# Kernel optimization log

Hardware: AMD Instinct MI355X
Metric: run time of the kernel (lower is better)

Reference implementation:

```python
import jax, jax.numpy as jnp
import numpy as np

N_RAYS = 4096
N_SAMPLES = 128
NEAR, FAR = 0.5, 4.0
BOX_MIN, BOX_MAX = -4.0, 4.0
N_LEVELS = 16
F_PER_LEVEL = 2
LOG2_T = 19
LOW_RES, HIGH_RES = 16.0, 512.0
GEO_FEAT = 15
HIDDEN = 64
HIDDEN_C = 64
IN_CH = N_LEVELS * F_PER_LEVEL      # 32 hash-grid features
IN_CH_VIEWS = 16                     # SH degree 4
OUT_CH = 4                           # 3 color channels + sigma (last)
N_APP = 64
APP_DIM = 16

PRIMES = np.array([1, 2654435761, 805459861], dtype=np.uint32)
OFFSETS = np.array([[i, j, k] for i in (0, 1) for j in (0, 1) for k in (0, 1)], dtype=np.int32)  # [8,3]

C0 = 0.28209479177387814
C1 = 0.4886025119029199
C2 = (1.0925484305920792, -1.0925484305920792, 0.31539156525252005, -1.0925484305920792, 0.5462742152960396)
C3 = (-0.5900435899266435, 2.890611442640554, -0.4570457994644658, 0.3731763325901154, -0.4570457994644658, 1.445305721320277, -0.5900435899266435)


def sh_encode(d):
    x, y, z = d[..., 0], d[..., 1], d[..., 2]
    xx, yy, zz = x * x, y * y, z * z
    xy, yz, xz = x * y, y * z, x * z
    return jnp.stack([
        C0 * jnp.ones_like(x),
        -C1 * y, C1 * z, -C1 * x,
        C2[0] * xy, C2[1] * yz, C2[2] * (2 * zz - xx - yy), C2[3] * xz, C2[4] * (xx - yy),
        C3[0] * y * (3 * xx - yy), C3[1] * xy * z, C3[2] * y * (4 * zz - xx - yy),
        C3[3] * z * (2 * zz - 3 * xx - 3 * yy), C3[4] * x * (4 * zz - xx - yy),
        C3[5] * z * (xx - yy), C3[6] * x * (xx - 3 * yy)], axis=-1)


def hash_encode(x, tables):
    # x: [N,3]; tables: [L, 2^T, F]. Multi-res hash grid with trilinear interp (Instant-NGP / HashNeRF).
    keep = jnp.all((x >= BOX_MIN) & (x <= BOX_MAX), axis=-1)
    xc = jnp.clip(x, BOX_MIN, BOX_MAX)
    b = np.exp((np.log(HIGH_RES) - np.log(LOW_RES)) / (N_LEVELS - 1))
    resolutions = jnp.asarray(np.floor(LOW_RES * b ** np.arange(N_LEVELS)), dtype=jnp.float32)
    hmask = jnp.uint32(2 ** LOG2_T - 1)
    primes = jnp.asarray(PRIMES)
    off = jnp.asarray(OFFSETS)
    off_u = off.astype(jnp.uint32)

    def level(args):
        table, res = args
        grid = (BOX_MAX - BOX_MIN) / res
        pos = (xc - BOX_MIN) / grid
        bl = jnp.floor(pos)
        frac = pos - bl                                    # [N,3]
        corners = bl.astype(jnp.uint32)[:, None, :] + off_u[None]  # [N,8,3]
        h = corners * primes                               # uint32 wraparound
        idx = (h[..., 0] ^ h[..., 1] ^ h[..., 2]) & hmask  # [N,8]
        emb = table[idx]                                   # [N,8,F]
        w = jnp.stack([1.0 - frac, frac], axis=-1)         # [N,3,2]
        cw = w[:, 0, off[:, 0]] * w[:, 1, off[:, 1]] * w[:, 2, off[:, 2]]  # [N,8]
        return jnp.einsum('nc,ncf->nf', cw, emb)           # [N,F]

    feats = jax.lax.map(level, (tables, resolutions))      # [L,N,F]
    feats = jnp.transpose(feats, (1, 0, 2)).reshape(x.shape[0], -1)
    return feats, keep


def _forward(rays, hash_tables, w_s0, w_s1, w_s2, w_c0, w_c1, w_c2, w_c3, app_table):
    R = rays.shape[0]
    rays_o, rays_d = rays[:, :3], rays[:, 3:6]
    codes = rays[:, 6].astype(jnp.int32)
    z = jnp.linspace(NEAR, FAR, N_SAMPLES)
    zvals = jax.lax.stop_gradient(jnp.broadcast_to(z, (R, N_SAMPLES)))
    samples = jax.lax.stop_gradient(rays_o[:, None, :] + rays_d[:, None, :] * z[None, :, None])  # [R,S,3]
    viewdirs = jax.lax.stop_gradient(jnp.broadcast_to(rays_d[:, None, :], (R, N_SAMPLES, 3)))

    pts = samples.reshape(-1, 3)
    dirs = viewdirs.reshape(-1, 3)
    enc_p, keep = hash_encode(pts, hash_tables)            # [N,32], [N]
    enc_d = sh_encode(dirs)                                # [N,16]

    # sigma network (bias-free, HashNeRF NeRFSmall)
    h = jax.nn.relu(enc_p @ w_s0)
    h = jax.nn.relu(h @ w_s1)
    h = h @ w_s2                                           # [N, 1+geo_feat]
    sigma = h[:, :1]
    geo = h[:, 1:]

    # color network with per-ray appearance embedding
    app = app_table[jnp.repeat(codes, N_SAMPLES)]          # [N, APP_DIM]
    c = jnp.concatenate([enc_d, geo, app], axis=-1)
    c = jax.nn.relu(c @ w_c0)
    c = jax.nn.relu(c @ w_c1)
    c = jax.nn.relu(c @ w_c2)
    c = c @ w_c3                                           # [N, OUT_CH-1]

    sigma = jnp.where(keep[:, None], sigma, 0.0)           # output[~keep_mask, -1] = 0
    raw = jnp.concatenate([c, sigma], axis=-1).reshape(R, N_SAMPLES, OUT_CH)

    # volumetric integration
    dists = jnp.concatenate([zvals[:, 1:] - zvals[:, :-1], jnp.full((R, 1), 1e10)], axis=-1)
    dists = dists * jnp.linalg.norm(rays_d, axis=-1, keepdims=True)
    sig = jax.nn.relu(raw[..., -1])
    alpha = 1.0 - jnp.exp(-sig * dists)
    trans = jnp.cumprod(jnp.concatenate([jnp.ones((R, 1)), 1.0 - alpha + 1e-10], axis=-1), axis=-1)[:, :-1]
    weights = alpha * trans                                # [R,S]
    chs = jax.nn.sigmoid(raw[..., :-1])
    chs_map = jnp.einsum('rs,rsc->rc', weights, chs)       # [R, OUT_CH-1]
    depth_map = jnp.sum(weights * zvals, axis=-1)          # [R]
    p = jnp.concatenate([weights, 1.0 - jnp.sum(weights, -1, keepdims=True) + 1e-6], axis=-1)
    p = jnp.clip(p, 1e-12, None)
    p = p / jnp.sum(p, -1, keepdims=True)
    sparsity_loss = -jnp.sum(p * jnp.log(p), axis=-1)      # [R] Categorical entropy
    return chs_map, depth_map, sparsity_loss


def setup_inputs() -> dict:
    key = jax.random.key(0)
    ks = jax.random.split(key, 12)
    rays_o = jax.random.uniform(ks[0], (N_RAYS, 3), minval=-0.5, maxval=0.5)
    d = jax.random.normal(ks[1], (N_RAYS, 3))
    rays_d = d / jnp.linalg.norm(d, axis=-1, keepdims=True)
    codes = jax.random.randint(ks[2], (N_RAYS, 1), 0, N_APP).astype(jnp.float32)
    rays = jnp.concatenate([rays_o, rays_d, codes], axis=-1)  # [R,7]
    hash_tables = (jax.random.uniform(ks[3], (N_LEVELS, 2 ** LOG2_T, F_PER_LEVEL)) * 2.0 - 1.0) * 1e-4
    def init_w(k, shape):
        return jax.random.normal(k, shape) * (1.0 / np.sqrt(shape[0]))
    w_s0 = init_w(ks[4], (IN_CH, HIDDEN))
    w_s1 = init_w(ks[5], (HIDDEN, HIDDEN))
    w_s2 = init_w(ks[6], (HIDDEN, 1 + GEO_FEAT))
    c_in = IN_CH_VIEWS + GEO_FEAT + APP_DIM
    w_c0 = init_w(ks[7], (c_in, HIDDEN_C))
    w_c1 = init_w(ks[8], (HIDDEN_C, HIDDEN_C))
    w_c2 = init_w(ks[9], (HIDDEN_C, HIDDEN_C))
    w_c3 = init_w(ks[10], (HIDDEN_C, OUT_CH - 1))
    app_table = jax.random.normal(ks[11], (N_APP, APP_DIM)) * 0.01
    return {"rays": rays, "app_code": 0, "hash_tables": hash_tables,
            "w_s0": w_s0, "w_s1": w_s1, "w_s2": w_s2,
            "w_c0": w_c0, "w_c1": w_c1, "w_c2": w_c2, "w_c3": w_c3,
            "app_table": app_table}


def reference(rays, app_code, hash_tables, w_s0, w_s1, w_s2, w_c0, w_c1, w_c2, w_c3, app_table):
    # app_code arg is ignored by the original forward (it re-reads rays[:, 6]).
    return _forward(rays, hash_tables, w_s0, w_s1, w_s2, w_c0, w_c1, w_c2, w_c3, app_table)
```

## Files before the change

kernel.cpp:

```cpp
#include <hip/hip_runtime.h>
#include <math.h>

typedef unsigned short u16;
typedef short bf16x8 __attribute__((ext_vector_type(8)));
typedef float f32x4 __attribute__((ext_vector_type(4)));

#define NRAYS 4096
#define NSAMP 128
#define NPTS (NRAYS * NSAMP)
#define TBL_MASK 0x7FFFFu
#define LVL_STRIDE (524288 * 2)

#define SB_W0H 0
#define SB_W0M 2048
#define SB_W0L 4096
#define SB_W1H 6144
#define SB_W1M 10240
#define SB_W1L 14336
#define WB_G   18432
#define WB_C0  19456
#define WB_C1  23552
#define WB_C2  27648
#define WB_C3  31744
#define RAW_OFF 131072

#define MEMBAR() asm volatile("" ::: "memory")

struct ResArr { float r[16]; };

__device__ __forceinline__ u16 f2b(float f) {
  unsigned u = __float_as_uint(f);
  unsigned r = u + 0x7FFFu + ((u >> 16) & 1u);
  return (u16)(r >> 16);
}
__device__ __forceinline__ unsigned pack2(float lo, float hi) {
  return (unsigned)f2b(lo) | ((unsigned)f2b(hi) << 16);
}
__device__ __forceinline__ float b2f(u16 u) {
  return __uint_as_float(((unsigned)u) << 16);
}
__device__ __forceinline__ void split3(float x, u16& h, u16& m, u16& l) {
  h = f2b(x);
  float r = x - b2f(h);
  m = f2b(r);
  l = f2b(r - b2f(m));
}
__device__ __forceinline__ void split8(float4 a, float4 b, bf16x8* S) {
  float v[8] = {a.x, a.y, a.z, a.w, b.x, b.y, b.z, b.w};
  #pragma unroll
  for (int e = 0; e < 8; ++e) {
    u16 h, m, l; split3(v[e], h, m, l);
    S[0][e] = (short)h; S[1][e] = (short)m; S[2][e] = (short)l;
  }
}
__device__ __forceinline__ bf16x8 tob8(float4 a, float4 b) {
  bf16x8 r;
  r[0] = (short)f2b(a.x); r[1] = (short)f2b(a.y); r[2] = (short)f2b(a.z); r[3] = (short)f2b(a.w);
  r[4] = (short)f2b(b.x); r[5] = (short)f2b(b.y); r[6] = (short)f2b(b.z); r[7] = (short)f2b(b.w);
  return r;
}
__device__ __forceinline__ float sigmoidf_(float x) { return 1.f / (1.f + expf(-x)); }

__global__ void __launch_bounds__(256)
prep_kernel(const float* __restrict__ ws0, const float* __restrict__ ws1,
            const float* __restrict__ ws2, const float* __restrict__ wc0,
            const float* __restrict__ wc1, const float* __restrict__ wc2,
            const float* __restrict__ wc3, u16* __restrict__ wb)
{
  __shared__ int P[32];
  __shared__ int Pinv[32];
  const int t = threadIdx.x;
  if (t < 64) {
    const int g = t >> 4;
    for (int tt = 0; tt < 32; ++tt) {
      bf16x8 A, B;
      #pragma unroll
      for (int e = 0; e < 8; ++e) {
        A[e] = (short)f2b((float)(g * 8 + e + 1));
        B[e] = (short)((g * 8 + e == tt) ? 0x3F80 : 0);
      }
      f32x4 c = {0.f, 0.f, 0.f, 0.f};
      c = __builtin_amdgcn_mfma_f32_16x16x32_bf16(A, B, c, 0, 0, 0);
      if (t == 0) P[tt] = (int)(c[0] + 0.5f) - 1;
    }
  }
  __syncthreads();
  if (t < 32) Pinv[t] = t;
  __syncthreads();
  if (t < 32) { int p = P[t]; if (p >= 0 && p < 32) Pinv[p] = t; }
  __syncthreads();

  for (int i = t; i < 2048; i += 256) {
    int o = i >> 5, k = i & 31, kt = Pinv[k];
    float v = ws0[kt * 64 + o];
    u16 h, m, l; split3(v, h, m, l);
    wb[SB_W0H + i] = h; wb[SB_W0M + i] = m; wb[SB_W0L + i] = l;
  }
  for (int i = t; i < 4096; i += 256) {
    int o = i >> 6, k = i & 63, kt = (k & 32) | Pinv[k & 31];
    float v = ws1[kt * 64 + o];
    u16 h, m, l; split3(v, h, m, l);
    wb[SB_W1H + i] = h; wb[SB_W1M + i] = m; wb[SB_W1L + i] = l;
  }
  for (int i = t; i < 1024; i += 256) {
    int o = i >> 6, s = i & 63, kt = (s & 32) | Pinv[s & 31];
    wb[WB_G + i] = f2b(ws2[kt * 16 + o]);
  }
  for (int i = t; i < 4096; i += 256) {
    int o = i >> 6, s = i & 63, kt = (s & 32) | Pinv[s & 31];
    float v = 0.f;
    if (kt < 16) v = wc0[kt * 64 + o];
    else if (kt >= 17 && kt <= 47) v = wc0[(kt - 1) * 64 + o];
    wb[WB_C0 + i] = f2b(v);
  }
  for (int i = t; i < 4096; i += 256) {
    int o = i >> 6, s = i & 63, kt = (s & 32) | Pinv[s & 31];
    wb[WB_C1 + i] = f2b(wc1[kt * 64 + o]);
  }
  for (int i = t; i < 4096; i += 256) {
    int o = i >> 6, s = i & 63, kt = (s & 32) | Pinv[s & 31];
    wb[WB_C2 + i] = f2b(wc2[kt * 64 + o]);
  }
  for (int i = t; i < 1024; i += 256) {
    int o = i >> 6, s = i & 63, kt = (s & 32) | Pinv[s & 31];
    wb[WB_C3 + i] = f2b(o < 3 ? wc3[kt * 3 + o] : 0.f);
  }
}

__global__ void __launch_bounds__(64, 2)
point_kernel(const float* __restrict__ rays, const float* __restrict__ tables,
             const u16* __restrict__ wb, const float* __restrict__ ws2,
             const float* __restrict__ app_table, u16* __restrict__ raw, ResArr RES)
{
  __shared__ char lds[16640];
  char* EC = lds;
  char* H1 = lds + 8192;
  char* H2 = lds + 12288;
  float* keepb = (float*)(lds + 16384);
  const int lane = threadIdx.x;
  const int pBase = blockIdx.x * 64;
  const int q = lane & 15, g = lane >> 4;
  const unsigned swzQ = (unsigned)((q & 7) << 4);
  const unsigned swzMy = (unsigned)((lane & 7) << 4);

  const int ptG = pBase + lane;
  const int r = ptG >> 7, s = ptG & (NSAMP - 1);
  const float ox = rays[r * 7 + 0], oy = rays[r * 7 + 1], oz = rays[r * 7 + 2];
  const float dx = rays[r * 7 + 3], dy = rays[r * 7 + 4], dz = rays[r * 7 + 5];
  const int code = (int)rays[r * 7 + 6];
  const float z = 0.5f + (3.5f / 127.f) * (float)s;
  const float x = fmaf(dx, z, ox), y = fmaf(dy, z, oy), w = fmaf(dz, z, oz);
  const bool keep = (x >= -4.f && x <= 4.f && y >= -4.f && y <= 4.f &&
                     w >= -4.f && w <= 4.f);
  const float xc = fminf(fmaxf(x, -4.f), 4.f);
  const float yc = fminf(fmaxf(y, -4.f), 4.f);
  const float zc = fminf(fmaxf(w, -4.f), 4.f);

  float encp[32];
  #pragma unroll
  for (int l = 0; l < 16; ++l) {
    const float res = RES.r[l];
    const float sc = res * 0.125f;
    const float px = (xc + 4.f) * sc, py = (yc + 4.f) * sc, pz = (zc + 4.f) * sc;
    const float bx = floorf(px), by = floorf(py), bz = floorf(pz);
    const float fx = px - bx, fy = py - by, fz = pz - bz;
    const unsigned ix = (unsigned)bx, iy = (unsigned)by, iz = (unsigned)bz;
    const unsigned hx0 = ix, hx1 = ix + 1u;
    const unsigned hy0 = iy * 2654435761u, hy1 = (iy + 1u) * 2654435761u;
    const unsigned hz0 = iz * 805459861u,  hz1 = (iz + 1u) * 805459861u;
    const float wx0 = 1.f - fx, wy0 = 1.f - fy, wz0 = 1.f - fz;
    const float* tl = tables + (size_t)l * LVL_STRIDE;
    float f0 = 0.f, f1 = 0.f;
    #pragma unroll
    for (int c = 0; c < 8; ++c) {
      const unsigned cx = (c >> 2) & 1, cy = (c >> 1) & 1, cz = c & 1;
      const unsigned idx = ((cx ? hx1 : hx0) ^ (cy ? hy1 : hy0) ^ (cz ? hz1 : hz0)) & TBL_MASK;
      const float cw = (cx ? fx : wx0) * (cy ? fy : wy0) * (cz ? fz : wz0);
      const float2 e = *reinterpret_cast<const float2*>(tl + (size_t)idx * 2);
      f0 = fmaf(cw, e.x, f0);
      f1 = fmaf(cw, e.y, f1);
    }
    encp[2 * l] = f0;
    encp[2 * l + 1] = f1;
  }
  #pragma unroll
  for (int c = 0; c < 8; ++c) {
    float4 u = make_float4(encp[4 * c + 0], encp[4 * c + 1], encp[4 * c + 2], encp[4 * c + 3]);
    *(float4*)(EC + lane * 128 + (((unsigned)(c * 16)) ^ swzMy)) = u;
  }
  keepb[lane] = keep ? 1.f : 0.f;
  MEMBAR();

  auto six = [&](const u16* ph, const u16* pm, const u16* pl,
                 bf16x8 bh, bf16x8 bm, bf16x8 bl, f32x4 c) -> f32x4 {
    bf16x8 Ah = *(const bf16x8*)ph, Am = *(const bf16x8*)pm, Al = *(const bf16x8*)pl;
    c = __builtin_amdgcn_mfma_f32_16x16x32_bf16(Ah, bh, c, 0, 0, 0);
    c = __builtin_amdgcn_mfma_f32_16x16x32_bf16(Am, bh, c, 0, 0, 0);
    c = __builtin_amdgcn_mfma_f32_16x16x32_bf16(Al, bh, c, 0, 0, 0);
    c = __builtin_amdgcn_mfma_f32_16x16x32_bf16(Ah, bm, c, 0, 0, 0);
    c = __builtin_amdgcn_mfma_f32_16x16x32_bf16(Am, bm, c, 0, 0, 0);
    c = __builtin_amdgcn_mfma_f32_16x16x32_bf16(Ah, bl, c, 0, 0, 0);
    return c;
  };

  float sigv[4];
  #pragma unroll
  for (int n = 0; n < 4; ++n) {
    bf16x8 B0[3];
    {
      const char* p = EC + (n * 16 + q) * 128;
      float4 a = *(const float4*)(p + (((unsigned)(g * 32)) ^ swzQ));
      float4 b = *(const float4*)(p + (((unsigned)(g * 32 + 16)) ^ swzQ));
      split8(a, b, B0);
    }
    #pragma unroll
    for (int m = 0; m < 4; ++m) {
      const int row = (m * 16 + q) * 32 + g * 8;
      f32x4 c = {0.f, 0.f, 0.f, 0.f};
      c = six(wb + SB_W0H + row, wb + SB_W0M + row, wb + SB_W0L + row,
              B0[0], B0[1], B0[2], c);
      c[0] = fmaxf(c[0], 0.f); c[1] = fmaxf(c[1], 0.f);
      c[2] = fmaxf(c[2], 0.f); c[3] = fmaxf(c[3], 0.f);
      float4 st = make_float4(c[0], c[1], c[2], c[3]);
      *(float4*)(H1 + q * 256 + (((unsigned)(m * 64 + g * 16)) ^ swzQ)) = st;
    }
    MEMBAR();

    bf16x8 B1a[3], B1b[3];
    {
      const char* p = H1 + q * 256;
      float4 a0 = *(const float4*)(p + (((unsigned)(g * 32)) ^ swzQ));
      float4 b0 = *(const float4*)(p + (((unsigned)(g * 32 + 16)) ^ swzQ));
      split8(a0, b0, B1a);
      float4 a1 = *(const float4*)(p + (((unsigned)(128 + g * 32)) ^ swzQ));
      float4 b1 = *(const float4*)(p + (((unsigned)(128 + g * 32 + 16)) ^ swzQ));
      split8(a1, b1, B1b);
    }
    #pragma unroll
    for (int m = 0; m < 4; ++m) {
      const int r0 = (m * 16 + q) * 64 + g * 8;
      const int r1 = r0 + 32;
      f32x4 c = {0.f, 0.f, 0.f, 0.f};
      c = six(wb + SB_W1H + r0, wb + SB_W1M + r0, wb + SB_W1L + r0,
              B1a[0], B1a[1], B1a[2], c);
      c = six(wb + SB_W1H + r1, wb + SB_W1M + r1, wb + SB_W1L + r1,
              B1b[0], B1b[1], B1b[2], c);
      c[0] = fmaxf(c[0], 0.f); c[1] = fmaxf(c[1], 0.f);
      c[2] = fmaxf(c[2], 0.f); c[3] = fmaxf(c[3], 0.f);
      float4 st = make_float4(c[0], c[1], c[2], c[3]);
      *(float4*)(H2 + q * 256 + (((unsigned)(m * 64 + g * 16)) ^ swzQ)) = st;
    }
    MEMBAR();

    {
      const char* p = H2 + q * 256;
      float4 a0 = *(const float4*)(p + (((unsigned)(g * 32)) ^ swzQ));
      float4 b0 = *(const float4*)(p + (((unsigned)(g * 32 + 16)) ^ swzQ));
      bf16x8 Bg0 = tob8(a0, b0);
      float4 a1 = *(const float4*)(p + (((unsigned)(128 + g * 32)) ^ swzQ));
      float4 b1 = *(const float4*)(p + (((unsigned)(128 + g * 32 + 16)) ^ swzQ));
      bf16x8 Bg1 = tob8(a1, b1);
      bf16x8 A0 = *(const bf16x8*)(wb + WB_G + q * 64 + g * 8);
      bf16x8 A1 = *(const bf16x8*)(wb + WB_G + q * 64 + 32 + g * 8);
      f32x4 cg = {0.f, 0.f, 0.f, 0.f};
      cg = __builtin_amdgcn_mfma_f32_16x16x32_bf16(A0, Bg0, cg, 0, 0, 0);
      cg = __builtin_amdgcn_mfma_f32_16x16x32_bf16(A1, Bg1, cg, 0, 0, 0);
      uint2 u; u.x = pack2(cg[0], cg[1]); u.y = pack2(cg[2], cg[3]);
      *(uint2*)(EC + (n * 16 + q) * 128 + (((unsigned)(32 + 8 * g)) ^ swzQ)) = u;
    }
    {
      float sp = 0.f;
      #pragma unroll
      for (int j4 = 0; j4 < 4; ++j4) {
        float4 h = *(const float4*)(H2 + q * 256 + (((unsigned)(g * 64 + j4 * 16)) ^ swzQ));
        const int ch = g * 16 + j4 * 4;
        sp = fmaf(h.x, ws2[(ch + 0) * 16], sp);
        sp = fmaf(h.y, ws2[(ch + 1) * 16], sp);
        sp = fmaf(h.z, ws2[(ch + 2) * 16], sp);
        sp = fmaf(h.w, ws2[(ch + 3) * 16], sp);
      }
      sp += __shfl_xor(sp, 16);
      sp += __shfl_xor(sp, 32);
      sigv[n] = sp * keepb[n * 16 + q];
    }
    MEMBAR();
  }

  {
    const float xx = dx * dx, yy = dy * dy, zz2 = dz * dz;
    const float xy = dx * dy, yz = dy * dz, xz = dx * dz;
    float e0 = 0.28209479177387814f;
    float e1 = -0.4886025119029199f * dy;
    float e2 = 0.4886025119029199f * dz;
    float e3 = -0.4886025119029199f * dx;
    float e4 = 1.0925484305920792f * xy;
    float e5 = -1.0925484305920792f * yz;
    float e6 = 0.31539156525252005f * (2.f * zz2 - xx - yy);
    float e7 = -1.0925484305920792f * xz;
    float e8 = 0.5462742152960396f * (xx - yy);
    float e9 = -0.5900435899266435f * dy * (3.f * xx - yy);
    float e10 = 2.890611442640554f * xy * dz;
    float e11 = -0.4570457994644658f * dy * (4.f * zz2 - xx - yy);
    float e12 = 0.3731763325901154f * dz * (2.f * zz2 - 3.f * xx - 3.f * yy);
    float e13 = -0.4570457994644658f * dx * (4.f * zz2 - xx - yy);
    float e14 = 1.445305721320277f * dz * (xx - yy);
    float e15 = -0.5900435899266435f * dx * (xx - 3.f * yy);
    uint4 u0; u0.x = pack2(e0, e1);  u0.y = pack2(e2, e3);  u0.z = pack2(e4, e5);  u0.w = pack2(e6, e7);
    uint4 u1; u1.x = pack2(e8, e9);  u1.y = pack2(e10, e11); u1.z = pack2(e12, e13); u1.w = pack2(e14, e15);
    *(uint4*)(EC + lane * 128 + (0u ^ swzMy)) = u0;
    *(uint4*)(EC + lane * 128 + (16u ^ swzMy)) = u1;
    const float4* ap = (const float4*)(app_table + (size_t)code * 16);
    float4 a0 = ap[0], a1 = ap[1], a2 = ap[2], a3 = ap[3];
    uint4 v0; v0.x = pack2(a0.x, a0.y); v0.y = pack2(a0.z, a0.w); v0.z = pack2(a1.x, a1.y); v0.w = pack2(a1.z, a1.w);
    uint4 v1; v1.x = pack2(a2.x, a2.y); v1.y = pack2(a2.z, a2.w); v1.z = pack2(a3.x, a3.y); v1.w = pack2(a3.z, a3.w);
    *(uint4*)(EC + lane * 128 + (64u ^ swzMy)) = v0;
    *(uint4*)(EC + lane * 128 + (80u ^ swzMy)) = v1;
    uint4 zv; zv.x = 0u; zv.y = 0u; zv.z = 0u; zv.w = 0u;
    *(uint4*)(EC + lane * 128 + (96u ^ swzMy)) = zv;
    *(uint4*)(EC + lane * 128 + (112u ^ swzMy)) = zv;
  }
  MEMBAR();

  auto rdB = [&](int n, int kc) -> bf16x8 {
    return *(const bf16x8*)(EC + (n * 16 + q) * 128 + (((unsigned)(kc * 64 + g * 16)) ^ swzQ));
  };
  auto ldA = [&](const u16* Wp, int row, int kc) -> bf16x8 {
    return *(const bf16x8*)(Wp + row * 64 + kc * 32 + g * 8);
  };
  auto wrC = [&](int n, int slot0, f32x4 c) {
    c[0] = fmaxf(c[0], 0.f); c[1] = fmaxf(c[1], 0.f);
    c[2] = fmaxf(c[2], 0.f); c[3] = fmaxf(c[3], 0.f);
    uint2 u; u.x = pack2(c[0], c[1]); u.y = pack2(c[2], c[3]);
    *(uint2*)(EC + (n * 16 + q) * 128 + (((unsigned)(slot0 * 2)) ^ swzQ)) = u;
  };
  auto layer64 = [&](const u16* Wp) {
    bf16x8 A[4][2];
    #pragma unroll
    for (int m = 0; m < 4; ++m) {
      A[m][0] = ldA(Wp, m * 16 + q, 0);
      A[m][1] = ldA(Wp, m * 16 + q, 1);
    }
    #pragma unroll
    for (int n = 0; n < 4; ++n) {
      bf16x8 b0 = rdB(n, 0), b1 = rdB(n, 1);
      #pragma unroll
      for (int m = 0; m < 4; ++m) {
        f32x4 c = {0.f, 0.f, 0.f, 0.f};
        c = __builtin_amdgcn_mfma_f32_16x16x32_bf16(A[m][0], b0, c, 0, 0, 0);
        c = __builtin_amdgcn_mfma_f32_16x16x32_bf16(A[m][1], b1, c, 0, 0, 0);
        wrC(n, m * 16 + g * 4, c);
      }
    }
    MEMBAR();
  };

  layer64(wb + WB_C0);
  layer64(wb + WB_C1);
  layer64(wb + WB_C2);

  {
    const u16* Wp = wb + WB_C3;
    bf16x8 A0 = ldA(Wp, q, 0), A1 = ldA(Wp, q, 1);
    #pragma unroll
    for (int n = 0; n < 4; ++n) {
      bf16x8 b0 = rdB(n, 0), b1 = rdB(n, 1);
      f32x4 c = {0.f, 0.f, 0.f, 0.f};
      c = __builtin_amdgcn_mfma_f32_16x16x32_bf16(A0, b0, c, 0, 0, 0);
      c = __builtin_amdgcn_mfma_f32_16x16x32_bf16(A1, b1, c, 0, 0, 0);
      if (g == 0) {
        uint2 o; o.x = pack2(c[0], c[1]); o.y = pack2(c[2], sigv[n]);
        *(uint2*)(raw + (size_t)(pBase + n * 16 + q) * 4) = o;
      }
    }
  }
}

__global__ void __launch_bounds__(256)
render_kernel(const float* __restrict__ rays, const u16* __restrict__ raw,
              float* __restrict__ out)
{
  const int r = blockIdx.x * 256 + threadIdx.x;
  if (r >= NRAYS) return;
  const float dx = rays[r * 7 + 3], dy = rays[r * 7 + 4], dz = rays[r * 7 + 5];
  const float nrm = sqrtf(dx * dx + dy * dy + dz * dz);
  const float dstep = 3.5f / 127.f;
  const ushort4* rp = reinterpret_cast<const ushort4*>(raw) + (size_t)r * NSAMP;

  float T = 1.f, sumw = 0.f, sumwz = 0.f, cm0 = 0.f, cm1 = 0.f, cm2 = 0.f;
  for (int s = 0; s < NSAMP; ++s) {
    const ushort4 rw = rp[s];
    const float dist = ((s < NSAMP - 1) ? dstep : 1e10f) * nrm;
    const float sigv = fmaxf(b2f(rw.w), 0.f);
    const float alpha = 1.f - expf(-sigv * dist);
    const float wgt = alpha * T;
    T *= (1.f - alpha + 1e-10f);
    const float zv = 0.5f + dstep * (float)s;
    sumw += wgt;
    sumwz = fmaf(wgt, zv, sumwz);
    cm0 = fmaf(wgt, sigmoidf_(b2f(rw.x)), cm0);
    cm1 = fmaf(wgt, sigmoidf_(b2f(rw.y)), cm1);
    cm2 = fmaf(wgt, sigmoidf_(b2f(rw.z)), cm2);
  }

  float S1 = 0.f, S2 = 0.f, T2 = 1.f;
  for (int s = 0; s < NSAMP; ++s) {
    const ushort4 rw = rp[s];
    const float dist = ((s < NSAMP - 1) ? dstep : 1e10f) * nrm;
    const float sigv = fmaxf(b2f(rw.w), 0.f);
    const float alpha = 1.f - expf(-sigv * dist);
    const float wgt = alpha * T2;
    T2 *= (1.f - alpha + 1e-10f);
    const float qv = fmaxf(wgt, 1e-12f);
    S1 += qv;
    S2 = fmaf(qv, logf(qv), S2);
  }
  const float plast = fmaxf(1.f - sumw + 1e-6f, 1e-12f);
  S1 += plast;
  S2 = fmaf(plast, logf(plast), S2);
  const float ent = logf(S1) - S2 / S1;

  out[r * 3 + 0] = cm0;
  out[r * 3 + 1] = cm1;
  out[r * 3 + 2] = cm2;
  out[NRAYS * 3 + r] = sumwz;
  out[NRAYS * 4 + r] = ent;
}

extern "C" void kernel_launch(void* const* d_in, const int* in_sizes, int n_in,
                              void* d_out, int out_size, void* d_ws, size_t ws_size,
                              hipStream_t stream)
{
  const float* rays   = (const float*)d_in[0];
  const float* tables = (const float*)d_in[2];
  const float* ws0    = (const float*)d_in[3];
  const float* ws1    = (const float*)d_in[4];
  const float* ws2    = (const float*)d_in[5];
  const float* wc0    = (const float*)d_in[6];
  const float* wc1    = (const float*)d_in[7];
  const float* wc2    = (const float*)d_in[8];
  const float* wc3    = (const float*)d_in[9];
  const float* app    = (const float*)d_in[10];

  u16* wb  = (u16*)d_ws;
  u16* raw = (u16*)((char*)d_ws + RAW_OFF);
  float* out = (float*)d_out;

  ResArr RES;
  const double b = exp((log(512.0) - log(16.0)) / 15.0);
  for (int l = 0; l < 16; ++l) RES.r[l] = (float)floor(16.0 * pow(b, (double)l));

  hipLaunchKernelGGL(prep_kernel, dim3(1), dim3(256), 0, stream,
                     ws0, ws1, ws2, wc0, wc1, wc2, wc3, wb);
  hipLaunchKernelGGL(point_kernel, dim3(NPTS / 64), dim3(64), 0, stream,
                     rays, tables, wb, ws2, app, raw, RES);
  hipLaunchKernelGGL(render_kernel, dim3(16), dim3(256), 0, stream,
                     rays, raw, out);
}
```

Baseline: 333.7 us.

## Use two-term bf16 split for density MLP, shrink LDS, spread prep and render work

```diff
diff --git a/kernel.cpp b/kernel.cpp
--- a/kernel.cpp
+++ b/kernel.cpp
@@ -11,17 +11,16 @@
 #define TBL_MASK 0x7FFFFu
 #define LVL_STRIDE (524288 * 2)
 
-#define SB_W0H 0
-#define SB_W0M 2048
-#define SB_W0L 4096
-#define SB_W1H 6144
-#define SB_W1M 10240
-#define SB_W1L 14336
-#define WB_G   18432
-#define WB_C0  19456
-#define WB_C1  23552
-#define WB_C2  27648
-#define WB_C3  31744
+#define W0H  0
+#define W0M  2048
+#define W1H  4096
+#define W1M  8192
+#define WBG  12288
+#define WBC0 13312
+#define WBC1 17408
+#define WBC2 21504
+#define WBC3 25600
+#define W2C0_OFF 57344
 #define RAW_OFF 131072
 
 #define MEMBAR() asm volatile("" ::: "memory")
@@ -39,18 +38,13 @@
 __device__ __forceinline__ float b2f(u16 u) {
   return __uint_as_float(((unsigned)u) << 16);
 }
-__device__ __forceinline__ void split3(float x, u16& h, u16& m, u16& l) {
-  h = f2b(x);
-  float r = x - b2f(h);
-  m = f2b(r);
-  l = f2b(r - b2f(m));
-}
-__device__ __forceinline__ void split8(float4 a, float4 b, bf16x8* S) {
+__device__ __forceinline__ void split2_8(float4 a, float4 b, bf16x8& H, bf16x8& M) {
   float v[8] = {a.x, a.y, a.z, a.w, b.x, b.y, b.z, b.w};
   #pragma unroll
   for (int e = 0; e < 8; ++e) {
-    u16 h, m, l; split3(v[e], h, m, l);
-    S[0][e] = (short)h; S[1][e] = (short)m; S[2][e] = (short)l;
+    u16 h = f2b(v[e]);
+    H[e] = (short)h;
+    M[e] = (short)f2b(v[e] - b2f(h));
   }
 }
 __device__ __forceinline__ bf16x8 tob8(float4 a, float4 b) {
@@ -65,7 +59,8 @@
 prep_kernel(const float* __restrict__ ws0, const float* __restrict__ ws1,
             const float* __restrict__ ws2, const float* __restrict__ wc0,
             const float* __restrict__ wc1, const float* __restrict__ wc2,
-            const float* __restrict__ wc3, u16* __restrict__ wb)
+            const float* __restrict__ wc3, u16* __restrict__ wb,
+            float* __restrict__ w2c0)
 {
   __shared__ int P[32];
   __shared__ int Pinv[32];
@@ -90,53 +85,54 @@
   if (t < 32) { int p = P[t]; if (p >= 0 && p < 32) Pinv[p] = t; }
   __syncthreads();
 
-  for (int i = t; i < 2048; i += 256) {
+  const int gt = blockIdx.x * 256 + t;
+  const int GS = 8 * 256;
+  for (int i = gt; i < 2048; i += GS) {
     int o = i >> 5, k = i & 31, kt = Pinv[k];
     float v = ws0[kt * 64 + o];
-    u16 h, m, l; split3(v, h, m, l);
-    wb[SB_W0H + i] = h; wb[SB_W0M + i] = m; wb[SB_W0L + i] = l;
-  }
-  for (int i = t; i < 4096; i += 256) {
+    u16 h = f2b(v);
+    wb[W0H + i] = h; wb[W0M + i] = f2b(v - b2f(h));
+  }
+  for (int i = gt; i < 4096; i += GS) {
     int o = i >> 6, k = i & 63, kt = (k & 32) | Pinv[k & 31];
     float v = ws1[kt * 64 + o];
-    u16 h, m, l; split3(v, h, m, l);
-    wb[SB_W1H + i] = h; wb[SB_W1M + i] = m; wb[SB_W1L + i] = l;
-  }
-  for (int i = t; i < 1024; i += 256) {
+    u16 h = f2b(v);
+    wb[W1H + i] = h; wb[W1M + i] = f2b(v - b2f(h));
+  }
+  for (int i = gt; i < 1024; i += GS) {
     int o = i >> 6, s = i & 63, kt = (s & 32) | Pinv[s & 31];
-    wb[WB_G + i] = f2b(ws2[kt * 16 + o]);
-  }
-  for (int i = t; i < 4096; i += 256) {
+    wb[WBG + i] = f2b(ws2[kt * 16 + o]);
+  }
+  for (int i = gt; i < 64; i += GS) w2c0[i] = ws2[i * 16];
+  for (int i = gt; i < 4096; i += GS) {
     int o = i >> 6, s = i & 63, kt = (s & 32) | Pinv[s & 31];
     float v = 0.f;
     if (kt < 16) v = wc0[kt * 64 + o];
     else if (kt >= 17 && kt <= 47) v = wc0[(kt - 1) * 64 + o];
-    wb[WB_C0 + i] = f2b(v);
-  }
-  for (int i = t; i < 4096; i += 256) {
+    wb[WBC0 + i] = f2b(v);
+  }
+  for (int i = gt; i < 4096; i += GS) {
     int o = i >> 6, s = i & 63, kt = (s & 32) | Pinv[s & 31];
-    wb[WB_C1 + i] = f2b(wc1[kt * 64 + o]);
-  }
-  for (int i = t; i < 4096; i += 256) {
+    wb[WBC1 + i] = f2b(wc1[kt * 64 + o]);
+  }
+  for (int i = gt; i < 4096; i += GS) {
     int o = i >> 6, s = i & 63, kt = (s & 32) | Pinv[s & 31];
-    wb[WB_C2 + i] = f2b(wc2[kt * 64 + o]);
-  }
-  for (int i = t; i < 1024; i += 256) {
+    wb[WBC2 + i] = f2b(wc2[kt * 64 + o]);
+  }
+  for (int i = gt; i < 1024; i += GS) {
     int o = i >> 6, s = i & 63, kt = (s & 32) | Pinv[s & 31];
-    wb[WB_C3 + i] = f2b(o < 3 ? wc3[kt * 3 + o] : 0.f);
-  }
-}
-
-__global__ void __launch_bounds__(64, 2)
+    wb[WBC3 + i] = f2b(o < 3 ? wc3[kt * 3 + o] : 0.f);
+  }
+}
+
+__global__ void __launch_bounds__(64, 4)
 point_kernel(const float* __restrict__ rays, const float* __restrict__ tables,
-             const u16* __restrict__ wb, const float* __restrict__ ws2,
+             const u16* __restrict__ wb, const float* __restrict__ w2c0,
              const float* __restrict__ app_table, u16* __restrict__ raw, ResArr RES)
 {
-  __shared__ char lds[16640];
+  __shared__ char lds[10240];
   char* EC = lds;
-  char* H1 = lds + 8192;
-  char* H2 = lds + 12288;
-  float* keepb = (float*)(lds + 16384);
+  char* HB = lds + 8192;
   const int lane = threadIdx.x;
   const int pBase = blockIdx.x * 64;
   const int q = lane & 15, g = lane >> 4;
@@ -152,6 +148,7 @@
   const float x = fmaf(dx, z, ox), y = fmaf(dy, z, oy), w = fmaf(dz, z, oz);
   const bool keep = (x >= -4.f && x <= 4.f && y >= -4.f && y <= 4.f &&
                      w >= -4.f && w <= 4.f);
+  const float keepf = keep ? 1.f : 0.f;
   const float xc = fminf(fmaxf(x, -4.f), 4.f);
   const float yc = fminf(fmaxf(y, -4.f), 4.f);
   const float zc = fminf(fmaxf(w, -4.f), 4.f);
@@ -188,101 +185,122 @@
     float4 u = make_float4(encp[4 * c + 0], encp[4 * c + 1], encp[4 * c + 2], encp[4 * c + 3]);
     *(float4*)(EC + lane * 128 + (((unsigned)(c * 16)) ^ swzMy)) = u;
   }
-  keepb[lane] = keep ? 1.f : 0.f;
   MEMBAR();
 
-  auto six = [&](const u16* ph, const u16* pm, const u16* pl,
-                 bf16x8 bh, bf16x8 bm, bf16x8 bl, f32x4 c) -> f32x4 {
-    bf16x8 Ah = *(const bf16x8*)ph, Am = *(const bf16x8*)pm, Al = *(const bf16x8*)pl;
+  auto four = [&](const u16* pH, const u16* pM, bf16x8 bh, bf16x8 bm, f32x4 c) -> f32x4 {
+    bf16x8 Ah = *(const bf16x8*)pH, Am = *(const bf16x8*)pM;
     c = __builtin_amdgcn_mfma_f32_16x16x32_bf16(Ah, bh, c, 0, 0, 0);
     c = __builtin_amdgcn_mfma_f32_16x16x32_bf16(Am, bh, c, 0, 0, 0);
-    c = __builtin_amdgcn_mfma_f32_16x16x32_bf16(Al, bh, c, 0, 0, 0);
     c = __builtin_amdgcn_mfma_f32_16x16x32_bf16(Ah, bm, c, 0, 0, 0);
     c = __builtin_amdgcn_mfma_f32_16x16x32_bf16(Am, bm, c, 0, 0, 0);
-    c = __builtin_amdgcn_mfma_f32_16x16x32_bf16(Ah, bl, c, 0, 0, 0);
     return c;
+  };
+  auto stH = [&](int mh, f32x4 c, bool relu) {
+    if (relu) {
+      c[0] = fmaxf(c[0], 0.f); c[1] = fmaxf(c[1], 0.f);
+      c[2] = fmaxf(c[2], 0.f); c[3] = fmaxf(c[3], 0.f);
+    }
+    *(float4*)(HB + q * 128 + (((unsigned)(mh * 64 + g * 16)) ^ swzQ)) =
+        make_float4(c[0], c[1], c[2], c[3]);
   };
 
   float sigv[4];
   #pragma unroll
   for (int n = 0; n < 4; ++n) {
-    bf16x8 B0[3];
+    bf16x8 B0h, B0m;
     {
       const char* p = EC + (n * 16 + q) * 128;
       float4 a = *(const float4*)(p + (((unsigned)(g * 32)) ^ swzQ));
       float4 b = *(const float4*)(p + (((unsigned)(g * 32 + 16)) ^ swzQ));
-      split8(a, b, B0);
-    }
-    #pragma unroll
-    for (int m = 0; m < 4; ++m) {
+      split2_8(a, b, B0h, B0m);
+    }
+    f32x4 acc1[4];
+    #pragma unroll
+    for (int m = 0; m < 4; ++m) acc1[m] = f32x4{0.f, 0.f, 0.f, 0.f};
+
+    #pragma unroll
+    for (int m = 0; m < 2; ++m) {
       const int row = (m * 16 + q) * 32 + g * 8;
       f32x4 c = {0.f, 0.f, 0.f, 0.f};
-      c = six(wb + SB_W0H + row, wb + SB_W0M + row, wb + SB_W0L + row,
-              B0[0], B0[1], B0[2], c);
-      c[0] = fmaxf(c[0], 0.f); c[1] = fmaxf(c[1], 0.f);
-      c[2] = fmaxf(c[2], 0.f); c[3] = fmaxf(c[3], 0.f);
-      float4 st = make_float4(c[0], c[1], c[2], c[3]);
-      *(float4*)(H1 + q * 256 + (((unsigned)(m * 64 + g * 16)) ^ swzQ)) = st;
-    }
-    MEMBAR();
-
-    bf16x8 B1a[3], B1b[3];
-    {
-      const char* p = H1 + q * 256;
-      float4 a0 = *(const float4*)(p + (((unsigned)(g * 32)) ^ swzQ));
-      float4 b0 = *(const float4*)(p + (((unsigned)(g * 32 + 16)) ^ swzQ));
-      split8(a0, b0, B1a);
-      float4 a1 = *(const float4*)(p + (((unsigned)(128 + g * 32)) ^ swzQ));
-      float4 b1 = *(const float4*)(p + (((unsigned)(128 + g * 32 + 16)) ^ swzQ));
-      split8(a1, b1, B1b);
+      c = four(wb + W0H + row, wb + W0M + row, B0h, B0m, c);
+      stH(m, c, true);
+    }
+    MEMBAR();
+    {
+      float4 a = *(const float4*)(HB + q * 128 + (((unsigned)(g * 32)) ^ swzQ));
+      float4 b = *(const float4*)(HB + q * 128 + (((unsigned)(g * 32 + 16)) ^ swzQ));
+      bf16x8 Bh, Bm; split2_8(a, b, Bh, Bm);
+      #pragma unroll
+      for (int m = 0; m < 4; ++m) {
+        const int row = (m * 16 + q) * 64 + g * 8;
+        acc1[m] = four(wb + W1H + row, wb + W1M + row, Bh, Bm, acc1[m]);
+      }
+    }
+    MEMBAR();
+    #pragma unroll
+    for (int m = 2; m < 4; ++m) {
+      const int row = (m * 16 + q) * 32 + g * 8;
+      f32x4 c = {0.f, 0.f, 0.f, 0.f};
+      c = four(wb + W0H + row, wb + W0M + row, B0h, B0m, c);
+      stH(m & 1, c, true);
+    }
+    MEMBAR();
+    {
+      float4 a = *(const float4*)(HB + q * 128 + (((unsigned)(g * 32)) ^ swzQ));
+      float4 b = *(const float4*)(HB + q * 128 + (((unsigned)(g * 32 + 16)) ^ swzQ));
+      bf16x8 Bh, Bm; split2_8(a, b, Bh, Bm);
+      #pragma unroll
+      for (int m = 0; m < 4; ++m) {
+        const int row = (m * 16 + q) * 64 + 32 + g * 8;
+        acc1[m] = four(wb + W1H + row, wb + W1M + row, Bh, Bm, acc1[m]);
+      }
     }
     #pragma unroll
     for (int m = 0; m < 4; ++m) {
-      const int r0 = (m * 16 + q) * 64 + g * 8;
-      const int r1 = r0 + 32;
-      f32x4 c = {0.f, 0.f, 0.f, 0.f};
-      c = six(wb + SB_W1H + r0, wb + SB_W1M + r0, wb + SB_W1L + r0,
-              B1a[0], B1a[1], B1a[2], c);
-      c = six(wb + SB_W1H + r1, wb + SB_W1M + r1, wb + SB_W1L + r1,
-              B1b[0], B1b[1], B1b[2], c);
-      c[0] = fmaxf(c[0], 0.f); c[1] = fmaxf(c[1], 0.f);
-      c[2] = fmaxf(c[2], 0.f); c[3] = fmaxf(c[3], 0.f);
-      float4 st = make_float4(c[0], c[1], c[2], c[3]);
-      *(float4*)(H2 + q * 256 + (((unsigned)(m * 64 + g * 16)) ^ swzQ)) = st;
-    }
-    MEMBAR();
-
-    {
-      const char* p = H2 + q * 256;
-      float4 a0 = *(const float4*)(p + (((unsigned)(g * 32)) ^ swzQ));
-      float4 b0 = *(const float4*)(p + (((unsigned)(g * 32 + 16)) ^ swzQ));
-      bf16x8 Bg0 = tob8(a0, b0);
-      float4 a1 = *(const float4*)(p + (((unsigned)(128 + g * 32)) ^ swzQ));
-      float4 b1 = *(const float4*)(p + (((unsigned)(128 + g * 32 + 16)) ^ swzQ));
-      bf16x8 Bg1 = tob8(a1, b1);
-      bf16x8 A0 = *(const bf16x8*)(wb + WB_G + q * 64 + g * 8);
-      bf16x8 A1 = *(const bf16x8*)(wb + WB_G + q * 64 + 32 + g * 8);
-      f32x4 cg = {0.f, 0.f, 0.f, 0.f};
-      cg = __builtin_amdgcn_mfma_f32_16x16x32_bf16(A0, Bg0, cg, 0, 0, 0);
-      cg = __builtin_amdgcn_mfma_f32_16x16x32_bf16(A1, Bg1, cg, 0, 0, 0);
-      uint2 u; u.x = pack2(cg[0], cg[1]); u.y = pack2(cg[2], cg[3]);
+      acc1[m][0] = fmaxf(acc1[m][0], 0.f); acc1[m][1] = fmaxf(acc1[m][1], 0.f);
+      acc1[m][2] = fmaxf(acc1[m][2], 0.f); acc1[m][3] = fmaxf(acc1[m][3], 0.f);
+    }
+    MEMBAR();
+    f32x4 gc = {0.f, 0.f, 0.f, 0.f};
+    float sp = 0.f;
+    stH(0, acc1[0], false); stH(1, acc1[1], false);
+    MEMBAR();
+    {
+      float4 a = *(const float4*)(HB + q * 128 + (((unsigned)(g * 32)) ^ swzQ));
+      float4 b = *(const float4*)(HB + q * 128 + (((unsigned)(g * 32 + 16)) ^ swzQ));
+      bf16x8 Bg = tob8(a, b);
+      gc = __builtin_amdgcn_mfma_f32_16x16x32_bf16(
+          *(const bf16x8*)(wb + WBG + q * 64 + g * 8), Bg, gc, 0, 0, 0);
+      float4 wa = *(const float4*)(w2c0 + g * 8);
+      float4 wb4 = *(const float4*)(w2c0 + g * 8 + 4);
+      sp = fmaf(a.x, wa.x, sp); sp = fmaf(a.y, wa.y, sp);
+      sp = fmaf(a.z, wa.z, sp); sp = fmaf(a.w, wa.w, sp);
+      sp = fmaf(b.x, wb4.x, sp); sp = fmaf(b.y, wb4.y, sp);
+      sp = fmaf(b.z, wb4.z, sp); sp = fmaf(b.w, wb4.w, sp);
+    }
+    MEMBAR();
+    stH(0, acc1[2], false); stH(1, acc1[3], false);
+    MEMBAR();
+    {
+      float4 a = *(const float4*)(HB + q * 128 + (((unsigned)(g * 32)) ^ swzQ));
+      float4 b = *(const float4*)(HB + q * 128 + (((unsigned)(g * 32 + 16)) ^ swzQ));
+      bf16x8 Bg = tob8(a, b);
+      gc = __builtin_amdgcn_mfma_f32_16x16x32_bf16(
+          *(const bf16x8*)(wb + WBG + q * 64 + 32 + g * 8), Bg, gc, 0, 0, 0);
+      float4 wa = *(const float4*)(w2c0 + 32 + g * 8);
+      float4 wb4 = *(const float4*)(w2c0 + 32 + g * 8 + 4);
+      sp = fmaf(a.x, wa.x, sp); sp = fmaf(a.y, wa.y, sp);
+      sp = fmaf(a.z, wa.z, sp); sp = fmaf(a.w, wa.w, sp);
+      sp = fmaf(b.x, wb4.x, sp); sp = fmaf(b.y, wb4.y, sp);
+      sp = fmaf(b.z, wb4.z, sp); sp = fmaf(b.w, wb4.w, sp);
+    }
+    {
+      uint2 u; u.x = pack2(gc[0], gc[1]); u.y = pack2(gc[2], gc[3]);
       *(uint2*)(EC + (n * 16 + q) * 128 + (((unsigned)(32 + 8 * g)) ^ swzQ)) = u;
     }
-    {
-      float sp = 0.f;
-      #pragma unroll
-      for (int j4 = 0; j4 < 4; ++j4) {
-        float4 h = *(const float4*)(H2 + q * 256 + (((unsigned)(g * 64 + j4 * 16)) ^ swzQ));
-        const int ch = g * 16 + j4 * 4;
-        sp = fmaf(h.x, ws2[(ch + 0) * 16], sp);
-        sp = fmaf(h.y, ws2[(ch + 1) * 16], sp);
-        sp = fmaf(h.z, ws2[(ch + 2) * 16], sp);
-        sp = fmaf(h.w, ws2[(ch + 3) * 16], sp);
-      }
-      sp += __shfl_xor(sp, 16);
-      sp += __shfl_xor(sp, 32);
-      sigv[n] = sp * keepb[n * 16 + q];
-    }
+    sp += __shfl_xor(sp, 16);
+    sp += __shfl_xor(sp, 32);
+    sigv[n] = sp * __shfl(keepf, n * 16 + q);
     MEMBAR();
   }
 
@@ -354,12 +372,12 @@
     MEMBAR();
   };
 
-  layer64(wb + WB_C0);
-  layer64(wb + WB_C1);
-  layer64(wb + WB_C2);
+  layer64(wb + WBC0);
+  layer64(wb + WBC1);
+  layer64(wb + WBC2);
 
   {
-    const u16* Wp = wb + WB_C3;
+    const u16* Wp = wb + WBC3;
     bf16x8 A0 = ldA(Wp, q, 0), A1 = ldA(Wp, q, 1);
     #pragma unroll
     for (int n = 0; n < 4; ++n) {
@@ -375,11 +393,11 @@
   }
 }
 
-__global__ void __launch_bounds__(256)
+__global__ void __launch_bounds__(64)
 render_kernel(const float* __restrict__ rays, const u16* __restrict__ raw,
               float* __restrict__ out)
 {
-  const int r = blockIdx.x * 256 + threadIdx.x;
+  const int r = blockIdx.x * 64 + threadIdx.x;
   if (r >= NRAYS) return;
   const float dx = rays[r * 7 + 3], dy = rays[r * 7 + 4], dz = rays[r * 7 + 5];
   const float nrm = sqrtf(dx * dx + dy * dy + dz * dz);
@@ -387,6 +405,7 @@
   const ushort4* rp = reinterpret_cast<const ushort4*>(raw) + (size_t)r * NSAMP;
 
   float T = 1.f, sumw = 0.f, sumwz = 0.f, cm0 = 0.f, cm1 = 0.f, cm2 = 0.f;
+  float S1 = 0.f, S2 = 0.f;
   for (int s = 0; s < NSAMP; ++s) {
     const ushort4 rw = rp[s];
     const float dist = ((s < NSAMP - 1) ? dstep : 1e10f) * nrm;
@@ -400,16 +419,6 @@
     cm0 = fmaf(wgt, sigmoidf_(b2f(rw.x)), cm0);
     cm1 = fmaf(wgt, sigmoidf_(b2f(rw.y)), cm1);
     cm2 = fmaf(wgt, sigmoidf_(b2f(rw.z)), cm2);
-  }
-
-  float S1 = 0.f, S2 = 0.f, T2 = 1.f;
-  for (int s = 0; s < NSAMP; ++s) {
-    const ushort4 rw = rp[s];
-    const float dist = ((s < NSAMP - 1) ? dstep : 1e10f) * nrm;
-    const float sigv = fmaxf(b2f(rw.w), 0.f);
-    const float alpha = 1.f - expf(-sigv * dist);
-    const float wgt = alpha * T2;
-    T2 *= (1.f - alpha + 1e-10f);
     const float qv = fmaxf(wgt, 1e-12f);
     S1 += qv;
     S2 = fmaf(qv, logf(qv), S2);
@@ -441,18 +450,19 @@
   const float* wc3    = (const float*)d_in[9];
   const float* app    = (const float*)d_in[10];
 
-  u16* wb  = (u16*)d_ws;
-  u16* raw = (u16*)((char*)d_ws + RAW_OFF);
+  u16* wb    = (u16*)d_ws;
+  float* w2c0 = (float*)((char*)d_ws + W2C0_OFF);
+  u16* raw   = (u16*)((char*)d_ws + RAW_OFF);
   float* out = (float*)d_out;
 
   ResArr RES;
   const double b = exp((log(512.0) - log(16.0)) / 15.0);
   for (int l = 0; l < 16; ++l) RES.r[l] = (float)floor(16.0 * pow(b, (double)l));
 
-  hipLaunchKernelGGL(prep_kernel, dim3(1), dim3(256), 0, stream,
-                     ws0, ws1, ws2, wc0, wc1, wc2, wc3, wb);
+  hipLaunchKernelGGL(prep_kernel, dim3(8), dim3(256), 0, stream,
+                     ws0, ws1, ws2, wc0, wc1, wc2, wc3, wb, w2c0);
   hipLaunchKernelGGL(point_kernel, dim3(NPTS / 64), dim3(64), 0, stream,
-                     rays, tables, wb, ws2, app, raw, RES);
-  hipLaunchKernelGGL(render_kernel, dim3(16), dim3(256), 0, stream,
+                     rays, tables, wb, w2c0, app, raw, RES);
+  hipLaunchKernelGGL(render_kernel, dim3(NRAYS / 64), dim3(64), 0, stream,
                      rays, raw, out);
 }
```

Result: faster. 322.2 us (-3.5%).
